# Kernel optimization log

Hardware: AMD Instinct MI355X
Metric: run time of the kernel (lower is better)

## Reference

```python
import math
import jax, jax.numpy as jnp
import numpy as np
from jax import lax


def _l2n(v, eps=1e-12):
    return v / (jnp.linalg.norm(v) + eps)


def _sn(w_bar, u, v):
    # one power iteration (as in SpectralNorm with power_iterations=1)
    h = w_bar.shape[0]
    wm = w_bar.reshape(h, -1)
    v = _l2n(wm.T @ u)
    u = _l2n(wm @ v)
    u = lax.stop_gradient(u)  # u, v are updated via .data in torch (no grad)
    v = lax.stop_gradient(v)
    sigma = u @ (wm @ v)
    return w_bar / sigma


def _conv(x, w, stride, pad):
    return lax.conv_general_dilated(
        x, w, (stride, stride), [(pad, pad), (pad, pad)],
        dimension_numbers=('NCHW', 'OIHW', 'NCHW'))


def _make_blur_kernel():
    k = jnp.array([1., 3., 3., 1.], jnp.float32)
    k2 = k[None, :] * k[:, None]
    return k2 / k2.sum()  # 4x4, sums to 1


def _blur(x, k2, pad):
    # upfirdn2d with up=1, down=1: pad then depthwise FIR filter
    C = x.shape[1]
    xp = jnp.pad(x, ((0, 0), (0, 0), (pad[0], pad[1]), (pad[0], pad[1])))
    w = jnp.tile(k2[None, None], (C, 1, 1, 1))  # [C,1,4,4]
    return lax.conv_general_dilated(
        xp, w, (1, 1), 'VALID', feature_group_count=C,
        dimension_numbers=('NCHW', 'OIHW', 'NCHW'))


def setup_inputs() -> dict:
    key = jax.random.key(0)
    ks = jax.random.split(key, 12)
    Cin, Cout = 256, 512
    x = jax.random.normal(ks[0], (16, Cin, 64, 64), jnp.float32)
    w1_bar = jax.random.normal(ks[1], (Cin, Cin, 3, 3), jnp.float32) * 0.05
    u1 = _l2n(jax.random.normal(ks[2], (Cin,), jnp.float32))
    v1 = _l2n(jax.random.normal(ks[3], (Cin * 9,), jnp.float32))
    b1 = jnp.zeros((Cin,), jnp.float32)
    w2_bar = jax.random.normal(ks[4], (Cout, Cin, 3, 3), jnp.float32) * 0.05
    u2 = _l2n(jax.random.normal(ks[5], (Cout,), jnp.float32))
    v2 = _l2n(jax.random.normal(ks[6], (Cin * 9,), jnp.float32))
    b2 = jnp.zeros((Cout,), jnp.float32)
    ws_bar = jax.random.normal(ks[7], (Cout, Cin, 1, 1), jnp.float32) * 0.05
    us = _l2n(jax.random.normal(ks[8], (Cout,), jnp.float32))
    vs = _l2n(jax.random.normal(ks[9], (Cin,), jnp.float32))
    return dict(x=x, w1_bar=w1_bar, u1=u1, v1=v1, b1=b1,
                w2_bar=w2_bar, u2=u2, v2=v2, b2=b2,
                ws_bar=ws_bar, us=us, vs=vs)


def reference(x, w1_bar, u1, v1, b1, w2_bar, u2, v2, b2, ws_bar, us, vs):
    k2 = _make_blur_kernel()
    # conv1: 3x3 same-res, SN conv + bias + LeakyReLU(0.2)
    out = _conv(x, _sn(w1_bar, u1, v1), 1, 1) + b1[None, :, None, None]
    out = jax.nn.leaky_relu(out, 0.2)
    # conv2: blur pad=(2,2) then 3x3 stride-2 SN conv + bias + LeakyReLU
    out = _blur(out, k2, (2, 2))
    out = _conv(out, _sn(w2_bar, u2, v2), 2, 0) + b2[None, :, None, None]
    out = jax.nn.leaky_relu(out, 0.2)
    # skip: blur pad=(1,1) then 1x1 stride-2 SN conv (no bias, no act)
    skip = _blur(x, k2, (1, 1))
    skip = _conv(skip, _sn(ws_bar, us, vs), 2, 0)
    return (out + skip) / math.sqrt(2)
```

## Files before the change

### kernel.cpp

```cpp
#include <hip/hip_runtime.h>
#include <math.h>

typedef unsigned short u16;
typedef __attribute__((ext_vector_type(8))) unsigned short ushort8;
typedef __attribute__((ext_vector_type(4))) unsigned short u16x4;
typedef __attribute__((ext_vector_type(8))) short short8;
typedef __attribute__((ext_vector_type(4))) float f32x4;

__device__ __forceinline__ float b2f(u16 v) {
    unsigned u = ((unsigned)v) << 16; float f; __builtin_memcpy(&f, &u, 4); return f;
}
__device__ __forceinline__ u16 f2b(float f) {
    unsigned u; __builtin_memcpy(&u, &f, 4);
    u = (u + 0x7fffu + ((u >> 16) & 1u)) >> 16;
    return (u16)u;
}
__device__ __forceinline__ float ldin(const void* p, int i, int flag) {
    return flag ? ((const float*)p)[i] : b2f(((const u16*)p)[i]);
}
__device__ __forceinline__ void split2(float x, u16& h, u16& l) {
    h = f2b(x);
    l = f2b(x - b2f(h));
}
__device__ __forceinline__ ushort8 zero8() {
    ushort8 z;
#pragma unroll
    for (int i = 0; i < 8; ++i) z[i] = 0;
    return z;
}

__global__ void detect_kernel(const unsigned* __restrict__ xw, int* __restrict__ flag) {
    __shared__ int red[4];
    int tid = threadIdx.x, lane = tid & 63, wid = tid >> 6;
    int cnt = 0;
    for (int i = 0; i < 16; ++i) {
        unsigned w = xw[tid * 16 + i];
        unsigned e = (w >> 23) & 0xFF;
        if (e >= 77u && e <= 157u) ++cnt;
    }
    for (int o = 32; o; o >>= 1) cnt += __shfl_down(cnt, o, 64);
    if (lane == 0) red[wid] = cnt;
    __syncthreads();
    if (tid == 0) flag[0] = (red[0] + red[1] + red[2] + red[3] >= 2048) ? 1 : 0;
}

__global__ void sig_init_kernel(float* __restrict__ t, float* __restrict__ ns) {
    int i = blockIdx.x * 256 + threadIdx.x;
    if (i < 4864) t[i] = 0.f;
    if (i < 3) ns[i] = 0.f;
}

__global__ void sig_t_kernel(const void* __restrict__ w1, const void* __restrict__ u1,
                             const void* __restrict__ w2, const void* __restrict__ u2,
                             const void* __restrict__ wsb, const void* __restrict__ us,
                             const int* __restrict__ flagp, float* __restrict__ t) {
    __shared__ float ush[64];
    int blk = blockIdx.x;
    int flag = flagp[0];
    const void* W; const void* U; int m, toff, jc, ic;
    if (blk < 36)       { W = w1;  U = u1; m = 2304; toff = 0;    jc = blk % 9; ic = blk / 9; }
    else if (blk < 108) { int r = blk - 36;  W = w2;  U = u2; m = 2304; toff = 2304; jc = r % 9; ic = r / 9; }
    else                { int r = blk - 108; W = wsb; U = us; m = 256;  toff = 4608; jc = 0;     ic = r; }
    int tid = threadIdx.x;
    if (tid < 64) ush[tid] = ldin(U, ic * 64 + tid, flag);
    __syncthreads();
    int j = jc * 256 + tid;
    float acc = 0.f;
    int base = ic * 64 * m + j;
    for (int ii = 0; ii < 64; ++ii) acc += ldin(W, base + ii * m, flag) * ush[ii];
    atomicAdd(&t[toff + j], acc);
}

__global__ void sig_norm_kernel(float* __restrict__ t, float* __restrict__ ntinv) {
    __shared__ float red[4];
    int b = blockIdx.x;
    int m = (b == 2) ? 256 : 2304;
    int toff = b * 2304;
    int tid = threadIdx.x, lane = tid & 63, wid = tid >> 6;
    float s = 0.f;
    for (int j = tid; j < m; j += 256) { float v = t[toff + j]; s += v * v; }
    for (int o = 32; o; o >>= 1) s += __shfl_down(s, o, 64);
    if (lane == 0) red[wid] = s;
    __syncthreads();
    if (tid == 0) ntinv[b] = 1.f / (sqrtf(red[0] + red[1] + red[2] + red[3]) + 1e-12f);
}

__global__ void sig_s_kernel(const void* __restrict__ w1, const void* __restrict__ w2,
                             const void* __restrict__ wsb, const int* __restrict__ flagp,
                             const float* __restrict__ t, const float* __restrict__ ntinv,
                             float* __restrict__ ns) {
    int flag = flagp[0];
    int wg = blockIdx.x * 4 + (threadIdx.x >> 6);
    int lane = threadIdx.x & 63;
    const void* W; int m, toff, i, b;
    if (wg < 256)      { W = w1;  m = 2304; toff = 0;    i = wg;       b = 0; }
    else if (wg < 768) { W = w2;  m = 2304; toff = 2304; i = wg - 256; b = 1; }
    else               { W = wsb; m = 256;  toff = 4608; i = wg - 768; b = 2; }
    float acc = 0.f;
    int base = i * m;
    for (int j = lane; j < m; j += 64) acc += ldin(W, base + j, flag) * t[toff + j];
    for (int o = 32; o; o >>= 1) acc += __shfl_down(acc, o, 64);
    if (lane == 0) { float s = acc * ntinv[b]; atomicAdd(&ns[b], s * s); }
}

__global__ void sig_fin_kernel(const float* __restrict__ ns, float* __restrict__ inv_sigma) {
    int b = threadIdx.x;
    if (b < 3) { float s2 = ns[b]; float s = sqrtf(s2); inv_sigma[b] = (s + 1e-12f) / s2; }
}

__global__ void wprep_kernel(const void* __restrict__ w1b, const void* __restrict__ w2b,
                             const void* __restrict__ wsb,
                             const void* __restrict__ b1,  const void* __restrict__ b2,
                             const float* __restrict__ inv_sigma, const int* __restrict__ flagp,
                             u16* __restrict__ w1h, u16* __restrict__ w1l,
                             u16* __restrict__ w2h, u16* __restrict__ w2l,
                             u16* __restrict__ wsh, u16* __restrict__ wsl,
                             float* __restrict__ b1f, float* __restrict__ b2f_) {
    int idx = blockIdx.x * 256 + threadIdx.x;
    int flag = flagp[0];
    float s0 = inv_sigma[0], s1 = inv_sigma[1], s2 = inv_sigma[2];
    if (idx < 589824) {
        int kyx = idx / 65536; int rem = idx - kyx * 65536;
        int co = rem >> 8, ci = rem & 255;
        float w = ldin(w1b, ((co << 8) + ci) * 9 + kyx, flag) * s0;
        split2(w, w1h[idx], w1l[idx]);
    } else if (idx < 589824 + 1179648) {
        int i2 = idx - 589824;
        int kyx = i2 / 131072; int rem = i2 - kyx * 131072;
        int co = rem >> 8, ci = rem & 255;
        float w = ldin(w2b, ((co << 8) + ci) * 9 + kyx, flag) * s1;
        split2(w, w2h[i2], w2l[i2]);
    } else if (idx < 1900544) {
        int i3 = idx - 1769472;
        float w = ldin(wsb, i3, flag) * s2;
        split2(w, wsh[i3], wsl[i3]);
    } else if (idx < 1900544 + 256) {
        b1f[idx - 1900544] = ldin(b1, idx - 1900544, flag);
    } else if (idx < 1900544 + 768) {
        b2f_[idx - 1900800] = ldin(b2, idx - 1900800, flag);
    }
}

__global__ void transpose_kernel(const void* __restrict__ x, u16* __restrict__ xh,
                                 u16* __restrict__ xl,
                                 const int* __restrict__ flagp, int n0) {
    __shared__ float tile[32][65];
    int flag = flagp[0];
    int ny  = blockIdx.x;
    int ci0 = blockIdx.y * 32;
    int nl = ny >> 6, y = ny & 63;
    int t = threadIdx.x;
    int ci_l = t >> 3, x8 = (t & 7) * 8;
    int base = ((n0 + nl) * 256 + ci0 + ci_l) * 4096 + y * 64 + x8;
#pragma unroll
    for (int k = 0; k < 8; ++k) tile[ci_l][x8 + k] = ldin(x, base + k, flag);
    __syncthreads();
    int x_l = t >> 2, oc = (t & 3) * 8;
    size_t o = ((size_t)ny * 64 + x_l) * 256 + ci0 + oc;
    ushort8 h, l;
#pragma unroll
    for (int k = 0; k < 8; ++k) {
        u16 hh, ll; split2(tile[oc + k][x_l], hh, ll);
        h[k] = hh; l[k] = ll;
    }
    *(ushort8*)&xh[o] = h;
    *(ushort8*)&xl[o] = l;
}

__device__ __constant__ float BW[4] = {0.125f, 0.375f, 0.375f, 0.125f};

__global__ void blur1_kernel(const float* __restrict__ act1, u16* __restrict__ bh,
                             u16* __restrict__ bl) {
    int idx = blockIdx.x * 256 + threadIdx.x;
    int q = (idx & 63) * 4;
    int rem = idx >> 6;
    int xq = rem % 65; rem /= 65;
    int yq = rem % 65;
    int n  = rem / 65;
    float4 acc = {0.f, 0.f, 0.f, 0.f};
#pragma unroll
    for (int i = 0; i < 4; ++i) {
        int yy = yq + i - 2;
        if ((unsigned)yy >= 64u) continue;
#pragma unroll
        for (int j = 0; j < 4; ++j) {
            int xx = xq + j - 2;
            if ((unsigned)xx >= 64u) continue;
            float w = BW[i] * BW[j];
            float4 v = *(const float4*)&act1[((size_t)((n * 64 + yy) * 64 + xx) << 8) + q];
            acc.x += w * v.x; acc.y += w * v.y; acc.z += w * v.z; acc.w += w * v.w;
        }
    }
    u16x4 h, l;
    u16 hh, ll;
    split2(acc.x, hh, ll); h[0] = hh; l[0] = ll;
    split2(acc.y, hh, ll); h[1] = hh; l[1] = ll;
    split2(acc.z, hh, ll); h[2] = hh; l[2] = ll;
    split2(acc.w, hh, ll); h[3] = hh; l[3] = ll;
    *(u16x4*)&bh[(size_t)idx * 4] = h;
    *(u16x4*)&bl[(size_t)idx * 4] = l;
}

__global__ void blursample_kernel(const u16* __restrict__ xh, const u16* __restrict__ xl,
                                  u16* __restrict__ sh, u16* __restrict__ sl) {
    int idx = blockIdx.x * 256 + threadIdx.x;
    int q = (idx & 63) * 4;
    int rem = idx >> 6;
    int xo = rem & 31;
    int yo = (rem >> 5) & 31;
    int n  = rem >> 10;
    float4 acc = {0.f, 0.f, 0.f, 0.f};
#pragma unroll
    for (int i = 0; i < 4; ++i) {
        int yy = 2 * yo + i - 1;
        if ((unsigned)yy >= 64u) continue;
#pragma unroll
        for (int j = 0; j < 4; ++j) {
            int xx = 2 * xo + j - 1;
            if ((unsigned)xx >= 64u) continue;
            float w = BW[i] * BW[j];
            size_t g = ((size_t)((n * 64 + yy) * 64 + xx) << 8) + q;
            u16x4 vh = *(const u16x4*)&xh[g];
            u16x4 vl = *(const u16x4*)&xl[g];
            acc.x += w * (b2f(vh[0]) + b2f(vl[0]));
            acc.y += w * (b2f(vh[1]) + b2f(vl[1]));
            acc.z += w * (b2f(vh[2]) + b2f(vl[2]));
            acc.w += w * (b2f(vh[3]) + b2f(vl[3]));
        }
    }
    u16x4 h, l;
    u16 hh, ll;
    split2(acc.x, hh, ll); h[0] = hh; l[0] = ll;
    split2(acc.y, hh, ll); h[1] = hh; l[1] = ll;
    split2(acc.z, hh, ll); h[2] = hh; l[2] = ll;
    split2(acc.w, hh, ll); h[3] = hh; l[3] = ll;
    *(u16x4*)&sh[(size_t)idx * 4] = h;
    *(u16x4*)&sl[(size_t)idx * 4] = l;
}

#define LDK 40

template <bool DOLO>
__device__ __forceinline__ void conv1_body(
        const u16* __restrict__ xh, const u16* __restrict__ xl,
        const u16* __restrict__ w1h, const u16* __restrict__ w1l,
        const float* __restrict__ b1f, float* __restrict__ act1,
        u16* Ah, u16* Al, u16* Bh, u16* Bl) {
    int tid = threadIdx.x, lane = tid & 63, wid = tid >> 6;
    int col = lane & 15, quad = lane >> 4;
    int wco = (wid >> 1) * 64, wsp = (wid & 1) * 32;
    int bidx = blockIdx.x;
    int sp_blk = (bidx & 7) * 64 + (bidx >> 3);
    int sp_base = sp_blk * 64;
    int co_base = blockIdx.y * 128;
    int n  = sp_base >> 12;
    int y0 = (sp_base & 4095) >> 6;
    int ra = tid >> 1, ka = (tid & 1) * 16;
    int rb = tid >> 2, kb = (tid & 3) * 8;

    f32x4 acc[4][2];
#pragma unroll
    for (int i = 0; i < 4; ++i)
#pragma unroll
        for (int j = 0; j < 2; ++j) acc[i][j] = (f32x4){0.f, 0.f, 0.f, 0.f};

    for (int p = 0; p < 9; ++p) {
        int dy = p / 3 - 1, dx = p % 3 - 1;
        int yy = y0 + dy;
        if ((unsigned)yy >= 64u) continue;
        const u16* wh = w1h + (size_t)p * 65536;
        const u16* wl = w1l + (size_t)p * 65536;
        for (int kc = 0; kc < 8; ++kc) {
            int ci0 = kc * 32;
            __syncthreads();
            {
                size_t gs = (size_t)(co_base + ra) * 256 + ci0 + ka;
                *(ushort8*)&Ah[ra * LDK + ka]     = *(const ushort8*)&wh[gs];
                *(ushort8*)&Ah[ra * LDK + ka + 8] = *(const ushort8*)&wh[gs + 8];
                if (DOLO) {
                    *(ushort8*)&Al[ra * LDK + ka]     = *(const ushort8*)&wl[gs];
                    *(ushort8*)&Al[ra * LDK + ka + 8] = *(const ushort8*)&wl[gs + 8];
                }
            }
            {
                int xx = rb + dx;
                ushort8 h0, l0;
                if ((unsigned)xx < 64u) {
                    size_t g = ((size_t)((n * 64 + yy) * 64 + xx) << 8) + ci0 + kb;
                    h0 = *(const ushort8*)&xh[g];
                    if (DOLO) l0 = *(const ushort8*)&xl[g];
                } else {
                    h0 = zero8();
                    if (DOLO) l0 = zero8();
                }
                *(ushort8*)&Bh[rb * LDK + kb] = h0;
                if (DOLO) *(ushort8*)&Bl[rb * LDK + kb] = l0;
            }
            __syncthreads();
            short8 ah[4], al[4];
#pragma unroll
            for (int tm = 0; tm < 4; ++tm) {
                ah[tm] = *(const short8*)&Ah[(wco + tm * 16 + col) * LDK + quad * 8];
                if (DOLO) al[tm] = *(const short8*)&Al[(wco + tm * 16 + col) * LDK + quad * 8];
            }
#pragma unroll
            for (int tn = 0; tn < 2; ++tn) {
                short8 bh = *(const short8*)&Bh[(wsp + tn * 16 + col) * LDK + quad * 8];
                short8 bl;
                if (DOLO) bl = *(const short8*)&Bl[(wsp + tn * 16 + col) * LDK + quad * 8];
#pragma unroll
                for (int tm = 0; tm < 4; ++tm) {
                    acc[tm][tn] = __builtin_amdgcn_mfma_f32_16x16x32_bf16(ah[tm], bh, acc[tm][tn], 0, 0, 0);
                    if (DOLO) {
                        acc[tm][tn] = __builtin_amdgcn_mfma_f32_16x16x32_bf16(ah[tm], bl, acc[tm][tn], 0, 0, 0);
                        acc[tm][tn] = __builtin_amdgcn_mfma_f32_16x16x32_bf16(al[tm], bh, acc[tm][tn], 0, 0, 0);
                    }
                }
            }
        }
    }
#pragma unroll
    for (int tm = 0; tm < 4; ++tm) {
        int cog = co_base + wco + tm * 16 + quad * 4;
        float4 bias = *(const float4*)&b1f[cog];
#pragma unroll
        for (int tn = 0; tn < 2; ++tn) {
            int sp = sp_base + wsp + tn * 16 + col;
            float4 o;
            float v0 = acc[tm][tn][0] + bias.x; o.x = v0 > 0.f ? v0 : 0.2f * v0;
            float v1 = acc[tm][tn][1] + bias.y; o.y = v1 > 0.f ? v1 : 0.2f * v1;
            float v2 = acc[tm][tn][2] + bias.z; o.z = v2 > 0.f ? v2 : 0.2f * v2;
            float v3 = acc[tm][tn][3] + bias.w; o.w = v3 > 0.f ? v3 : 0.2f * v3;
            *(float4*)&act1[((size_t)sp << 8) + cog] = o;
        }
    }
}

__global__ __launch_bounds__(256, 4) void conv1_kernel(
        const u16* __restrict__ xh, const u16* __restrict__ xl,
        const u16* __restrict__ w1h, const u16* __restrict__ w1l,
        const float* __restrict__ b1f, float* __restrict__ act1,
        const int* __restrict__ flagp) {
    __shared__ u16 Ah[128 * LDK];
    __shared__ u16 Al[128 * LDK];
    __shared__ u16 Bh[64 * LDK];
    __shared__ u16 Bl[64 * LDK];
    if (flagp[0]) conv1_body<true >(xh, xl, w1h, w1l, b1f, act1, Ah, Al, Bh, Bl);
    else          conv1_body<false>(xh, xl, w1h, w1l, b1f, act1, Ah, Al, Bh, Bl);
}

template <bool DOLO>
__device__ __forceinline__ void conv2_body(
        const u16* __restrict__ bl1h, const u16* __restrict__ bl1l,
        const u16* __restrict__ skh,  const u16* __restrict__ skl,
        const u16* __restrict__ w2h, const u16* __restrict__ w2l,
        const u16* __restrict__ wsh, const u16* __restrict__ wsl,
        const float* __restrict__ b2f_, void* __restrict__ out, int n0,
        u16* Ah, u16* Al, u16* Bh, u16* Bl, int flag) {
    int tid = threadIdx.x, lane = tid & 63, wid = tid >> 6;
    int col = lane & 15, quad = lane >> 4;
    int wco = (wid >> 1) * 32, wsp = (wid & 1) * 64;
    int sp_base = blockIdx.x * 128;
    int co_base = blockIdx.y * 64;
    int n   = sp_base >> 10;
    int yo0 = (sp_base & 1023) >> 5;
    int r_st = tid >> 1, k_st = (tid & 1) * 16;
    int ra = tid >> 2, ka = (tid & 3) * 8;

    f32x4 acc[2][4], accs[2][4];
#pragma unroll
    for (int i = 0; i < 2; ++i)
#pragma unroll
        for (int j = 0; j < 4; ++j) {
            acc[i][j]  = (f32x4){0.f, 0.f, 0.f, 0.f};
            accs[i][j] = (f32x4){0.f, 0.f, 0.f, 0.f};
        }

    for (int p = 0; p < 10; ++p) {
        int ky = p / 3, kx = p % 3;
        const u16* wh = (p < 9) ? w2h + (size_t)p * 131072 : wsh;
        const u16* wl = (p < 9) ? w2l + (size_t)p * 131072 : wsl;
        for (int kc = 0; kc < 8; ++kc) {
            int ci0 = kc * 32;
            __syncthreads();
            {
                size_t gs = (size_t)(co_base + ra) * 256 + ci0 + ka;
                *(ushort8*)&Ah[ra * LDK + ka] = *(const ushort8*)&wh[gs];
                if (DOLO) *(ushort8*)&Al[ra * LDK + ka] = *(const ushort8*)&wl[gs];
            }
            {
                const u16 *srch, *srcl;
                size_t g;
                if (p < 9) {
                    int yi = 2 * (yo0 + (r_st >> 5)) + ky;
                    int xi = 2 * (r_st & 31) + kx;
                    g = (size_t)((n * 65 + yi) * 65 + xi) * 256 + ci0 + k_st;
                    srch = bl1h; srcl = bl1l;
                } else {
                    g = ((size_t)(sp_base + r_st) << 8) + ci0 + k_st;
                    srch = skh; srcl = skl;
                }
                *(ushort8*)&Bh[r_st * LDK + k_st]     = *(const ushort8*)&srch[g];
                *(ushort8*)&Bh[r_st * LDK + k_st + 8] = *(const ushort8*)&srch[g + 8];
                if (DOLO) {
                    *(ushort8*)&Bl[r_st * LDK + k_st]     = *(const ushort8*)&srcl[g];
                    *(ushort8*)&Bl[r_st * LDK + k_st + 8] = *(const ushort8*)&srcl[g + 8];
                }
            }
            __syncthreads();
            short8 ah[2], al[2];
#pragma unroll
            for (int tm = 0; tm < 2; ++tm) {
                ah[tm] = *(const short8*)&Ah[(wco + tm * 16 + col) * LDK + quad * 8];
                if (DOLO) al[tm] = *(const short8*)&Al[(wco + tm * 16 + col) * LDK + quad * 8];
            }
            if (p < 9) {
#pragma unroll
                for (int tn = 0; tn < 4; ++tn) {
                    short8 bh = *(const short8*)&Bh[(wsp + tn * 16 + col) * LDK + quad * 8];
                    short8 bl;
                    if (DOLO) bl = *(const short8*)&Bl[(wsp + tn * 16 + col) * LDK + quad * 8];
#pragma unroll
                    for (int tm = 0; tm < 2; ++tm) {
                        acc[tm][tn] = __builtin_amdgcn_mfma_f32_16x16x32_bf16(ah[tm], bh, acc[tm][tn], 0, 0, 0);
                        if (DOLO) {
                            acc[tm][tn] = __builtin_amdgcn_mfma_f32_16x16x32_bf16(ah[tm], bl, acc[tm][tn], 0, 0, 0);
                            acc[tm][tn] = __builtin_amdgcn_mfma_f32_16x16x32_bf16(al[tm], bh, acc[tm][tn], 0, 0, 0);
                        }
                    }
                }
            } else {
#pragma unroll
                for (int tn = 0; tn < 4; ++tn) {
                    short8 bh = *(const short8*)&Bh[(wsp + tn * 16 + col) * LDK + quad * 8];
                    short8 bl;
                    if (DOLO) bl = *(const short8*)&Bl[(wsp + tn * 16 + col) * LDK + quad * 8];
#pragma unroll
                    for (int tm = 0; tm < 2; ++tm) {
                        accs[tm][tn] = __builtin_amdgcn_mfma_f32_16x16x32_bf16(ah[tm], bh, accs[tm][tn], 0, 0, 0);
                        if (DOLO) {
                            accs[tm][tn] = __builtin_amdgcn_mfma_f32_16x16x32_bf16(ah[tm], bl, accs[tm][tn], 0, 0, 0);
                            accs[tm][tn] = __builtin_amdgcn_mfma_f32_16x16x32_bf16(al[tm], bh, accs[tm][tn], 0, 0, 0);
                        }
                    }
                }
            }
        }
    }
    const float RS2 = 0.70710678118654752f;
#pragma unroll
    for (int tm = 0; tm < 2; ++tm) {
        int cog = co_base + wco + tm * 16 + quad * 4;
        float4 bias = *(const float4*)&b2f_[cog];
        float bb[4] = {bias.x, bias.y, bias.z, bias.w};
#pragma unroll
        for (int tn = 0; tn < 4; ++tn) {
            int sp  = sp_base + wsp + tn * 16 + col;
            int ng  = n0 + (sp >> 10);
            int rem = sp & 1023;
            size_t ob = ((size_t)ng * 512 + cog) * 1024 + rem;
#pragma unroll
            for (int r = 0; r < 4; ++r) {
                float v = acc[tm][tn][r] + bb[r];
                v = v > 0.f ? v : 0.2f * v;
                v = (v + accs[tm][tn][r]) * RS2;
                if (flag) ((float*)out)[ob + (size_t)r * 1024] = v;
                else      ((u16*)out)[ob + (size_t)r * 1024]   = f2b(v);
            }
        }
    }
}

__global__ __launch_bounds__(256, 2) void conv2_kernel(
        const u16* __restrict__ bl1h, const u16* __restrict__ bl1l,
        const u16* __restrict__ skh,  const u16* __restrict__ skl,
        const u16* __restrict__ w2h, const u16* __restrict__ w2l,
        const u16* __restrict__ wsh, const u16* __restrict__ wsl,
        const float* __restrict__ b2f_, const int* __restrict__ flagp,
        void* __restrict__ out, int n0) {
    __shared__ u16 Ah[64 * LDK];
    __shared__ u16 Al[64 * LDK];
    __shared__ u16 Bh[128 * LDK];
    __shared__ u16 Bl[128 * LDK];
    int flag = flagp[0];
    if (flag) conv2_body<true >(bl1h, bl1l, skh, skl, w2h, w2l, wsh, wsl, b2f_, out, n0, Ah, Al, Bh, Bl, flag);
    else      conv2_body<false>(bl1h, bl1l, skh, skl, w2h, w2l, wsh, wsl, b2f_, out, n0, Ah, Al, Bh, Bl, flag);
}

extern "C" void kernel_launch(void* const* d_in, const int* in_sizes, int n_in,
                              void* d_out, int out_size, void* d_ws, size_t ws_size,
                              hipStream_t stream) {
    const void* x   = d_in[0];
    const void* w1b = d_in[1];
    const void* u1  = d_in[2];
    const void* b1  = d_in[4];
    const void* w2b = d_in[5];
    const void* u2  = d_in[6];
    const void* b2  = d_in[8];
    const void* wsb = d_in[9];
    const void* us  = d_in[10];

    char* ws = (char*)d_ws;
    int*   flag      = (int*)(ws);
    float* inv_sigma = (float*)(ws + 64);
    float* b1f       = (float*)(ws + 1024);
    float* b2fp      = (float*)(ws + 2048);
    u16* w1h = (u16*)(ws + 4096);
    u16* w1l = (u16*)(ws + 1183744);
    u16* w2h = (u16*)(ws + 2363392);
    u16* w2l = (u16*)(ws + 4722688);
    u16* wsh = (u16*)(ws + 7081984);
    u16* wsl = (u16*)(ws + 7344128);
    u16* xth  = (u16*)(ws + 7606272);
    u16* xtl  = (u16*)(ws + 7606272 + 16777216);
    u16* bl1h = (u16*)(ws + 7606272);
    u16* bl1l = (u16*)(ws + 7606272 + 17305600);
    float* act1 = (float*)(ws + 42217472);
    u16* skh = (u16*)(ws + 75771904);
    u16* skl = (u16*)(ws + 75771904 + 4194304);
    float* tvec  = (float*)(ws + 7606272);
    float* ntinv = (float*)(ws + 7606272 + 19456);
    float* ns    = (float*)(ws + 7606272 + 19520);

    detect_kernel<<<1, 256, 0, stream>>>((const unsigned*)x, flag);
    sig_init_kernel<<<19, 256, 0, stream>>>(tvec, ns);
    sig_t_kernel<<<116, 256, 0, stream>>>(w1b, u1, w2b, u2, wsb, us, flag, tvec);
    sig_norm_kernel<<<3, 256, 0, stream>>>(tvec, ntinv);
    sig_s_kernel<<<320, 256, 0, stream>>>(w1b, w2b, wsb, flag, tvec, ntinv, ns);
    sig_fin_kernel<<<1, 64, 0, stream>>>(ns, inv_sigma);
    wprep_kernel<<<7427, 256, 0, stream>>>(w1b, w2b, wsb, b1, b2, inv_sigma, flag,
                                           w1h, w1l, w2h, w2l, wsh, wsl, b1f, b2fp);
    for (int c = 0; c < 2; ++c) {
        int n0 = c * 8;
        transpose_kernel<<<dim3(512, 8), 256, 0, stream>>>(x, xth, xtl, flag, n0);
        blursample_kernel<<<2048, 256, 0, stream>>>(xth, xtl, skh, skl);
        conv1_kernel<<<dim3(512, 2), 256, 0, stream>>>(xth, xtl, w1h, w1l, b1f, act1, flag);
        blur1_kernel<<<8450, 256, 0, stream>>>(act1, bl1h, bl1l);
        conv2_kernel<<<dim3(64, 8), 256, 0, stream>>>(bl1h, bl1l, skh, skl, w2h, w2l,
                                                      wsh, wsl, b2fp, flag, d_out, n0);
    }
}
```

Baseline: 751.5 us.

## Prefetch next conv tiles into registers and store conv1 output as bf16 pairs

Conv1 and conv2 main loops are flattened into single iteration loops. The next iteration's global loads are issued into registers after the current LDS stores, so memory latency overlaps the MFMA work. Conv1's output is stored as split bf16 hi/lo pairs instead of fp32, and blur1 reconstructs the values from them. Conv1 no longer skips out-of-range rows; it zero-fills them, which adds some redundant MFMA work and register pressure.

Measured after the change: 744.6 us. About the same (-0.9%).

```diff
diff --git a/kernel.cpp b/kernel.cpp
--- a/kernel.cpp
+++ b/kernel.cpp
@@ -169,8 +169,8 @@
 
 __device__ __constant__ float BW[4] = {0.125f, 0.375f, 0.375f, 0.125f};
 
-__global__ void blur1_kernel(const float* __restrict__ act1, u16* __restrict__ bh,
-                             u16* __restrict__ bl) {
+__global__ void blur1_kernel(const u16* __restrict__ a1h, const u16* __restrict__ a1l,
+                             u16* __restrict__ bh, u16* __restrict__ bl) {
     int idx = blockIdx.x * 256 + threadIdx.x;
     int q = (idx & 63) * 4;
     int rem = idx >> 6;
@@ -187,8 +187,13 @@
             int xx = xq + j - 2;
             if ((unsigned)xx >= 64u) continue;
             float w = BW[i] * BW[j];
-            float4 v = *(const float4*)&act1[((size_t)((n * 64 + yy) * 64 + xx) << 8) + q];
-            acc.x += w * v.x; acc.y += w * v.y; acc.z += w * v.z; acc.w += w * v.w;
+            size_t g = ((size_t)((n * 64 + yy) * 64 + xx) << 8) + q;
+            u16x4 vh = *(const u16x4*)&a1h[g];
+            u16x4 vl = *(const u16x4*)&a1l[g];
+            acc.x += w * (b2f(vh[0]) + b2f(vl[0]));
+            acc.y += w * (b2f(vh[1]) + b2f(vl[1]));
+            acc.z += w * (b2f(vh[2]) + b2f(vl[2]));
+            acc.w += w * (b2f(vh[3]) + b2f(vl[3]));
         }
     }
     u16x4 h, l;
@@ -240,11 +245,29 @@
 
 #define LDK 40
 
+#define C1_LOAD(IT, RAH0, RAH1, RAL0, RAL1, RBH, RBL) {                        \
+    int p_ = (IT) >> 3, kc_ = (IT) & 7;                                        \
+    const u16* wh_ = w1h + (size_t)p_ * 65536;                                 \
+    const u16* wl_ = w1l + (size_t)p_ * 65536;                                 \
+    size_t gs_ = (size_t)(co_base + ra) * 256 + kc_ * 32 + ka;                 \
+    RAH0 = *(const ushort8*)&wh_[gs_];                                         \
+    RAH1 = *(const ushort8*)&wh_[gs_ + 8];                                     \
+    if (DOLO) { RAL0 = *(const ushort8*)&wl_[gs_];                             \
+                RAL1 = *(const ushort8*)&wl_[gs_ + 8]; }                       \
+    int dy_ = p_ / 3 - 1, dx_ = p_ % 3 - 1;                                    \
+    int yy_ = y0 + dy_, xx_ = rb + dx_;                                        \
+    if ((unsigned)yy_ < 64u && (unsigned)xx_ < 64u) {                          \
+        size_t g_ = ((size_t)((n * 64 + yy_) * 64 + xx_) << 8) + kc_ * 32 + kb;\
+        RBH = *(const ushort8*)&xh[g_];                                        \
+        if (DOLO) RBL = *(const ushort8*)&xl[g_];                              \
+    } else { RBH = zero8(); if (DOLO) RBL = zero8(); }                         \
+}
+
 template <bool DOLO>
 __device__ __forceinline__ void conv1_body(
         const u16* __restrict__ xh, const u16* __restrict__ xl,
         const u16* __restrict__ w1h, const u16* __restrict__ w1l,
-        const float* __restrict__ b1f, float* __restrict__ act1,
+        const float* __restrict__ b1f, u16* __restrict__ a1h, u16* __restrict__ a1l,
         u16* Ah, u16* Al, u16* Bh, u16* Bl) {
     int tid = threadIdx.x, lane = tid & 63, wid = tid >> 6;
     int col = lane & 15, quad = lane >> 4;
@@ -264,57 +287,39 @@
 #pragma unroll
         for (int j = 0; j < 2; ++j) acc[i][j] = (f32x4){0.f, 0.f, 0.f, 0.f};
 
-    for (int p = 0; p < 9; ++p) {
-        int dy = p / 3 - 1, dx = p % 3 - 1;
-        int yy = y0 + dy;
-        if ((unsigned)yy >= 64u) continue;
-        const u16* wh = w1h + (size_t)p * 65536;
-        const u16* wl = w1l + (size_t)p * 65536;
-        for (int kc = 0; kc < 8; ++kc) {
-            int ci0 = kc * 32;
-            __syncthreads();
-            {
-                size_t gs = (size_t)(co_base + ra) * 256 + ci0 + ka;
-                *(ushort8*)&Ah[ra * LDK + ka]     = *(const ushort8*)&wh[gs];
-                *(ushort8*)&Ah[ra * LDK + ka + 8] = *(const ushort8*)&wh[gs + 8];
+    ushort8 nAh0, nAh1, nAl0, nAl1, nBh, nBl;
+    C1_LOAD(0, nAh0, nAh1, nAl0, nAl1, nBh, nBl);
+
+    for (int it = 0; it < 72; ++it) {
+        __syncthreads();
+        *(ushort8*)&Ah[ra * LDK + ka]     = nAh0;
+        *(ushort8*)&Ah[ra * LDK + ka + 8] = nAh1;
+        if (DOLO) {
+            *(ushort8*)&Al[ra * LDK + ka]     = nAl0;
+            *(ushort8*)&Al[ra * LDK + ka + 8] = nAl1;
+        }
+        *(ushort8*)&Bh[rb * LDK + kb] = nBh;
+        if (DOLO) *(ushort8*)&Bl[rb * LDK + kb] = nBl;
+        int itn = (it + 1 < 72) ? it + 1 : it;
+        C1_LOAD(itn, nAh0, nAh1, nAl0, nAl1, nBh, nBl);
+        __syncthreads();
+        short8 ah[4], al[4];
+#pragma unroll
+        for (int tm = 0; tm < 4; ++tm) {
+            ah[tm] = *(const short8*)&Ah[(wco + tm * 16 + col) * LDK + quad * 8];
+            if (DOLO) al[tm] = *(const short8*)&Al[(wco + tm * 16 + col) * LDK + quad * 8];
+        }
+#pragma unroll
+        for (int tn = 0; tn < 2; ++tn) {
+            short8 bh = *(const short8*)&Bh[(wsp + tn * 16 + col) * LDK + quad * 8];
+            short8 bl;
+            if (DOLO) bl = *(const short8*)&Bl[(wsp + tn * 16 + col) * LDK + quad * 8];
+#pragma unroll
+            for (int tm = 0; tm < 4; ++tm) {
+                acc[tm][tn] = __builtin_amdgcn_mfma_f32_16x16x32_bf16(ah[tm], bh, acc[tm][tn], 0, 0, 0);
                 if (DOLO) {
-                    *(ushort8*)&Al[ra * LDK + ka]     = *(const ushort8*)&wl[gs];
-                    *(ushort8*)&Al[ra * LDK + ka + 8] = *(const ushort8*)&wl[gs + 8];
-                }
-            }
-            {
-                int xx = rb + dx;
-                ushort8 h0, l0;
-                if ((unsigned)xx < 64u) {
-                    size_t g = ((size_t)((n * 64 + yy) * 64 + xx) << 8) + ci0 + kb;
-                    h0 = *(const ushort8*)&xh[g];
-                    if (DOLO) l0 = *(const ushort8*)&xl[g];
-                } else {
-                    h0 = zero8();
-                    if (DOLO) l0 = zero8();
-                }
-                *(ushort8*)&Bh[rb * LDK + kb] = h0;
-                if (DOLO) *(ushort8*)&Bl[rb * LDK + kb] = l0;
-            }
-            __syncthreads();
-            short8 ah[4], al[4];
-#pragma unroll
-            for (int tm = 0; tm < 4; ++tm) {
-                ah[tm] = *(const short8*)&Ah[(wco + tm * 16 + col) * LDK + quad * 8];
-                if (DOLO) al[tm] = *(const short8*)&Al[(wco + tm * 16 + col) * LDK + quad * 8];
-            }
-#pragma unroll
-            for (int tn = 0; tn < 2; ++tn) {
-                short8 bh = *(const short8*)&Bh[(wsp + tn * 16 + col) * LDK + quad * 8];
-                short8 bl;
-                if (DOLO) bl = *(const short8*)&Bl[(wsp + tn * 16 + col) * LDK + quad * 8];
-#pragma unroll
-                for (int tm = 0; tm < 4; ++tm) {
-                    acc[tm][tn] = __builtin_amdgcn_mfma_f32_16x16x32_bf16(ah[tm], bh, acc[tm][tn], 0, 0, 0);
-                    if (DOLO) {
-                        acc[tm][tn] = __builtin_amdgcn_mfma_f32_16x16x32_bf16(ah[tm], bl, acc[tm][tn], 0, 0, 0);
-                        acc[tm][tn] = __builtin_amdgcn_mfma_f32_16x16x32_bf16(al[tm], bh, acc[tm][tn], 0, 0, 0);
-                    }
+                    acc[tm][tn] = __builtin_amdgcn_mfma_f32_16x16x32_bf16(ah[tm], bl, acc[tm][tn], 0, 0, 0);
+                    acc[tm][tn] = __builtin_amdgcn_mfma_f32_16x16x32_bf16(al[tm], bh, acc[tm][tn], 0, 0, 0);
                 }
             }
         }
@@ -323,15 +328,20 @@
     for (int tm = 0; tm < 4; ++tm) {
         int cog = co_base + wco + tm * 16 + quad * 4;
         float4 bias = *(const float4*)&b1f[cog];
+        float bb[4] = {bias.x, bias.y, bias.z, bias.w};
 #pragma unroll
         for (int tn = 0; tn < 2; ++tn) {
             int sp = sp_base + wsp + tn * 16 + col;
-            float4 o;
-            float v0 = acc[tm][tn][0] + bias.x; o.x = v0 > 0.f ? v0 : 0.2f * v0;
-            float v1 = acc[tm][tn][1] + bias.y; o.y = v1 > 0.f ? v1 : 0.2f * v1;
-            float v2 = acc[tm][tn][2] + bias.z; o.z = v2 > 0.f ? v2 : 0.2f * v2;
-            float v3 = acc[tm][tn][3] + bias.w; o.w = v3 > 0.f ? v3 : 0.2f * v3;
-            *(float4*)&act1[((size_t)sp << 8) + cog] = o;
+            u16x4 oh, ol;
+#pragma unroll
+            for (int r = 0; r < 4; ++r) {
+                float v = acc[tm][tn][r] + bb[r];
+                v = v > 0.f ? v : 0.2f * v;
+                u16 hh, ll; split2(v, hh, ll);
+                oh[r] = hh; ol[r] = ll;
+            }
+            *(u16x4*)&a1h[((size_t)sp << 8) + cog] = oh;
+            *(u16x4*)&a1l[((size_t)sp << 8) + cog] = ol;
         }
     }
 }
@@ -339,14 +349,38 @@
 __global__ __launch_bounds__(256, 4) void conv1_kernel(
         const u16* __restrict__ xh, const u16* __restrict__ xl,
         const u16* __restrict__ w1h, const u16* __restrict__ w1l,
-        const float* __restrict__ b1f, float* __restrict__ act1,
+        const float* __restrict__ b1f, u16* __restrict__ a1h, u16* __restrict__ a1l,
         const int* __restrict__ flagp) {
     __shared__ u16 Ah[128 * LDK];
     __shared__ u16 Al[128 * LDK];
     __shared__ u16 Bh[64 * LDK];
     __shared__ u16 Bl[64 * LDK];
-    if (flagp[0]) conv1_body<true >(xh, xl, w1h, w1l, b1f, act1, Ah, Al, Bh, Bl);
-    else          conv1_body<false>(xh, xl, w1h, w1l, b1f, act1, Ah, Al, Bh, Bl);
+    if (flagp[0]) conv1_body<true >(xh, xl, w1h, w1l, b1f, a1h, a1l, Ah, Al, Bh, Bl);
+    else          conv1_body<false>(xh, xl, w1h, w1l, b1f, a1h, a1l, Ah, Al, Bh, Bl);
+}
+
+#define C2_LOAD(IT, RAH, RAL, RBH0, RBH1, RBL0, RBL1) {                        \
+    int p_ = (IT) >> 3, kc_ = (IT) & 7; int ci0_ = kc_ * 32;                   \
+    const u16* wh_ = (p_ < 9) ? w2h + (size_t)p_ * 131072 : wsh;               \
+    const u16* wl_ = (p_ < 9) ? w2l + (size_t)p_ * 131072 : wsl;               \
+    size_t gs_ = (size_t)(co_base + ra) * 256 + ci0_ + ka;                     \
+    RAH = *(const ushort8*)&wh_[gs_];                                          \
+    if (DOLO) RAL = *(const ushort8*)&wl_[gs_];                                \
+    const u16 *sh_, *sl_; size_t g_;                                           \
+    if (p_ < 9) {                                                              \
+        int ky_ = p_ / 3, kx_ = p_ % 3;                                        \
+        int yi_ = 2 * (yo0 + (r_st >> 5)) + ky_;                               \
+        int xi_ = 2 * (r_st & 31) + kx_;                                       \
+        g_ = (size_t)((n * 65 + yi_) * 65 + xi_) * 256 + ci0_ + k_st;          \
+        sh_ = bl1h; sl_ = bl1l;                                                \
+    } else {                                                                   \
+        g_ = ((size_t)(sp_base + r_st) << 8) + ci0_ + k_st;                    \
+        sh_ = skh; sl_ = skl;                                                  \
+    }                                                                          \
+    RBH0 = *(const ushort8*)&sh_[g_];                                          \
+    RBH1 = *(const ushort8*)&sh_[g_ + 8];                                      \
+    if (DOLO) { RBL0 = *(const ushort8*)&sl_[g_];                              \
+                RBL1 = *(const ushort8*)&sl_[g_ + 8]; }                        \
 }
 
 template <bool DOLO>
@@ -376,72 +410,56 @@
             accs[i][j] = (f32x4){0.f, 0.f, 0.f, 0.f};
         }
 
-    for (int p = 0; p < 10; ++p) {
-        int ky = p / 3, kx = p % 3;
-        const u16* wh = (p < 9) ? w2h + (size_t)p * 131072 : wsh;
-        const u16* wl = (p < 9) ? w2l + (size_t)p * 131072 : wsl;
-        for (int kc = 0; kc < 8; ++kc) {
-            int ci0 = kc * 32;
-            __syncthreads();
-            {
-                size_t gs = (size_t)(co_base + ra) * 256 + ci0 + ka;
-                *(ushort8*)&Ah[ra * LDK + ka] = *(const ushort8*)&wh[gs];
-                if (DOLO) *(ushort8*)&Al[ra * LDK + ka] = *(const ushort8*)&wl[gs];
-            }
-            {
-                const u16 *srch, *srcl;
-                size_t g;
-                if (p < 9) {
-                    int yi = 2 * (yo0 + (r_st >> 5)) + ky;
-                    int xi = 2 * (r_st & 31) + kx;
-                    g = (size_t)((n * 65 + yi) * 65 + xi) * 256 + ci0 + k_st;
-                    srch = bl1h; srcl = bl1l;
-                } else {
-                    g = ((size_t)(sp_base + r_st) << 8) + ci0 + k_st;
-                    srch = skh; srcl = skl;
-                }
-                *(ushort8*)&Bh[r_st * LDK + k_st]     = *(const ushort8*)&srch[g];
-                *(ushort8*)&Bh[r_st * LDK + k_st + 8] = *(const ushort8*)&srch[g + 8];
-                if (DOLO) {
-                    *(ushort8*)&Bl[r_st * LDK + k_st]     = *(const ushort8*)&srcl[g];
-                    *(ushort8*)&Bl[r_st * LDK + k_st + 8] = *(const ushort8*)&srcl[g + 8];
+    ushort8 nAh, nAl, nBh0, nBh1, nBl0, nBl1;
+    C2_LOAD(0, nAh, nAl, nBh0, nBh1, nBl0, nBl1);
+
+    for (int it = 0; it < 80; ++it) {
+        int p = it >> 3;
+        __syncthreads();
+        *(ushort8*)&Ah[ra * LDK + ka] = nAh;
+        if (DOLO) *(ushort8*)&Al[ra * LDK + ka] = nAl;
+        *(ushort8*)&Bh[r_st * LDK + k_st]     = nBh0;
+        *(ushort8*)&Bh[r_st * LDK + k_st + 8] = nBh1;
+        if (DOLO) {
+            *(ushort8*)&Bl[r_st * LDK + k_st]     = nBl0;
+            *(ushort8*)&Bl[r_st * LDK + k_st + 8] = nBl1;
+        }
+        int itn = (it + 1 < 80) ? it + 1 : it;
+        C2_LOAD(itn, nAh, nAl, nBh0, nBh1, nBl0, nBl1);
+        __syncthreads();
+        short8 ah[2], al[2];
+#pragma unroll
+        for (int tm = 0; tm < 2; ++tm) {
+            ah[tm] = *(const short8*)&Ah[(wco + tm * 16 + col) * LDK + quad * 8];
+            if (DOLO) al[tm] = *(const short8*)&Al[(wco + tm * 16 + col) * LDK + quad * 8];
+        }
+        if (p < 9) {
+#pragma unroll
+            for (int tn = 0; tn < 4; ++tn) {
+                short8 bh = *(const short8*)&Bh[(wsp + tn * 16 + col) * LDK + quad * 8];
+                short8 bl;
+                if (DOLO) bl = *(const short8*)&Bl[(wsp + tn * 16 + col) * LDK + quad * 8];
+#pragma unroll
+                for (int tm = 0; tm < 2; ++tm) {
+                    acc[tm][tn] = __builtin_amdgcn_mfma_f32_16x16x32_bf16(ah[tm], bh, acc[tm][tn], 0, 0, 0);
+                    if (DOLO) {
+                        acc[tm][tn] = __builtin_amdgcn_mfma_f32_16x16x32_bf16(ah[tm], bl, acc[tm][tn], 0, 0, 0);
+                        acc[tm][tn] = __builtin_amdgcn_mfma_f32_16x16x32_bf16(al[tm], bh, acc[tm][tn], 0, 0, 0);
+                    }
                 }
             }
-            __syncthreads();
-            short8 ah[2], al[2];
-#pragma unroll
-            for (int tm = 0; tm < 2; ++tm) {
-                ah[tm] = *(const short8*)&Ah[(wco + tm * 16 + col) * LDK + quad * 8];
-                if (DOLO) al[tm] = *(const short8*)&Al[(wco + tm * 16 + col) * LDK + quad * 8];
-            }
-            if (p < 9) {
-#pragma unroll
-                for (int tn = 0; tn < 4; ++tn) {
-                    short8 bh = *(const short8*)&Bh[(wsp + tn * 16 + col) * LDK + quad * 8];
-                    short8 bl;
-                    if (DOLO) bl = *(const short8*)&Bl[(wsp + tn * 16 + col) * LDK + quad * 8];
-#pragma unroll
-                    for (int tm = 0; tm < 2; ++tm) {
-                        acc[tm][tn] = __builtin_amdgcn_mfma_f32_16x16x32_bf16(ah[tm], bh, acc[tm][tn], 0, 0, 0);
-                        if (DOLO) {
-                            acc[tm][tn] = __builtin_amdgcn_mfma_f32_16x16x32_bf16(ah[tm], bl, acc[tm][tn], 0, 0, 0);
-                            acc[tm][tn] = __builtin_amdgcn_mfma_f32_16x16x32_bf16(al[tm], bh, acc[tm][tn], 0, 0, 0);
-                        }
-                    }
-                }
-            } else {
-#pragma unroll
-                for (int tn = 0; tn < 4; ++tn) {
-                    short8 bh = *(const short8*)&Bh[(wsp + tn * 16 + col) * LDK + quad * 8];
-                    short8 bl;
-                    if (DOLO) bl = *(const short8*)&Bl[(wsp + tn * 16 + col) * LDK + quad * 8];
-#pragma unroll
-                    for (int tm = 0; tm < 2; ++tm) {
-                        accs[tm][tn] = __builtin_amdgcn_mfma_f32_16x16x32_bf16(ah[tm], bh, accs[tm][tn], 0, 0, 0);
-                        if (DOLO) {
-                            accs[tm][tn] = __builtin_amdgcn_mfma_f32_16x16x32_bf16(ah[tm], bl, accs[tm][tn], 0, 0, 0);
-                            accs[tm][tn] = __builtin_amdgcn_mfma_f32_16x16x32_bf16(al[tm], bh, accs[tm][tn], 0, 0, 0);
-                        }
+        } else {
+#pragma unroll
+            for (int tn = 0; tn < 4; ++tn) {
+                short8 bh = *(const short8*)&Bh[(wsp + tn * 16 + col) * LDK + quad * 8];
+                short8 bl;
+                if (DOLO) bl = *(const short8*)&Bl[(wsp + tn * 16 + col) * LDK + quad * 8];
+#pragma unroll
+                for (int tm = 0; tm < 2; ++tm) {
+                    accs[tm][tn] = __builtin_amdgcn_mfma_f32_16x16x32_bf16(ah[tm], bh, accs[tm][tn], 0, 0, 0);
+                    if (DOLO) {
+                        accs[tm][tn] = __builtin_amdgcn_mfma_f32_16x16x32_bf16(ah[tm], bl, accs[tm][tn], 0, 0, 0);
+                        accs[tm][tn] = __builtin_amdgcn_mfma_f32_16x16x32_bf16(al[tm], bh, accs[tm][tn], 0, 0, 0);
                     }
                 }
             }
@@ -515,7 +533,8 @@
     u16* xtl  = (u16*)(ws + 7606272 + 16777216);
     u16* bl1h = (u16*)(ws + 7606272);
     u16* bl1l = (u16*)(ws + 7606272 + 17305600);
-    float* act1 = (float*)(ws + 42217472);
+    u16* a1h = (u16*)(ws + 42217472);
+    u16* a1l = (u16*)(ws + 42217472 + 16777216);
     u16* skh = (u16*)(ws + 75771904);
     u16* skl = (u16*)(ws + 75771904 + 4194304);
     float* tvec  = (float*)(ws + 7606272);
@@ -534,8 +553,8 @@
         int n0 = c * 8;
         transpose_kernel<<<dim3(512, 8), 256, 0, stream>>>(x, xth, xtl, flag, n0);
         blursample_kernel<<<2048, 256, 0, stream>>>(xth, xtl, skh, skl);
-        conv1_kernel<<<dim3(512, 2), 256, 0, stream>>>(xth, xtl, w1h, w1l, b1f, act1, flag);
-        blur1_kernel<<<8450, 256, 0, stream>>>(act1, bl1h, bl1l);
+        conv1_kernel<<<dim3(512, 2), 256, 0, stream>>>(xth, xtl, w1h, w1l, b1f, a1h, a1l, flag);
+        blur1_kernel<<<8450, 256, 0, stream>>>(a1h, a1l, bl1h, bl1l);
         conv2_kernel<<<dim3(64, 8), 256, 0, stream>>>(bl1h, bl1l, skh, skl, w2h, w2l,
                                                       wsh, wsl, b2fp, flag, d_out, n0);
     }
```
